# Kernel optimization log

Hardware: AMD Instinct MI355X
Metric: run time of the kernel (lower is better)

## Reference

```python
import jax, jax.numpy as jnp
import numpy as np

B, S, D = 2, 4096, 256
H, DH, DM = 8, 32, 1024
ROPE_BASE = 10000.0
LN_EPS = 1e-5


def _layer_norm(x, g, b):
    mu = jnp.mean(x, axis=-1, keepdims=True)
    var = jnp.mean(jnp.square(x - mu), axis=-1, keepdims=True)
    return (x - mu) * jax.lax.rsqrt(var + LN_EPS) * g + b


def _rope(x):
    # x: [b, s, h, d_head]; lucidrains interleaved-pair RoPE
    s, d = x.shape[1], x.shape[-1]
    inv_freq = 1.0 / (ROPE_BASE ** (jnp.arange(0, d, 2, dtype=jnp.float32) / d))  # [d/2]
    freqs = jnp.arange(s, dtype=jnp.float32)[:, None] * inv_freq[None, :]          # [s, d/2]
    freqs = jnp.repeat(freqs, 2, axis=-1)                                          # [s, d]
    cos = jnp.cos(freqs)[None, :, None, :]
    sin = jnp.sin(freqs)[None, :, None, :]
    x1, x2 = x[..., 0::2], x[..., 1::2]
    rot = jnp.stack((-x2, x1), axis=-1).reshape(x.shape)
    return x * cos + rot * sin


def setup_inputs() -> dict:
    key = jax.random.key(0)
    ks = jax.random.split(key, 8)
    sw = 1.0 / np.sqrt(D)
    return {
        "x": jax.random.normal(ks[0], (B, S, D), jnp.float32),
        "Wq": jax.random.normal(ks[1], (D, D), jnp.float32) * sw,
        "Wk": jax.random.normal(ks[2], (D, D), jnp.float32) * sw,
        "Wv": jax.random.normal(ks[3], (D, D), jnp.float32) * sw,
        "Wo": jax.random.normal(ks[4], (D, D), jnp.float32) * sw,
        "ln1_g": jnp.ones((D,), jnp.float32),
        "ln1_b": jnp.zeros((D,), jnp.float32),
        "ln2_g": jnp.ones((D,), jnp.float32),
        "ln2_b": jnp.zeros((D,), jnp.float32),
        "W2": jax.random.normal(ks[5], (DM, D), jnp.float32) * sw,
        "b2": jnp.zeros((DM,), jnp.float32),
        "W3": jax.random.normal(ks[6], (D, DM), jnp.float32) * (1.0 / np.sqrt(DM)),
        "b3": jnp.zeros((D,), jnp.float32),
    }


def reference(x, Wq, Wk, Wv, Wo, ln1_g, ln1_b, ln2_g, ln2_b, W2, b2, W3, b3):
    b, s, d = x.shape
    h, dh = H, DH
    xn = _layer_norm(x, ln1_g, ln1_b)
    q = (xn @ Wq.T).reshape(b, s, h, dh)
    k = (xn @ Wk.T).reshape(b, s, h, dh)
    v = (xn @ Wv.T).reshape(b, s, h, dh)
    q = _rope(q)
    k = _rope(k)
    # scores: [b, h, q, k] (full matrix, matching original implementation)
    scores = jnp.einsum('bqhd,bkhd->bhqk', q, k) / np.sqrt(dh)
    attn = jax.nn.softmax(scores, axis=-1)
    out = jnp.einsum('bhqk,bkhd->bqhd', attn, v).reshape(b, s, d)
    out = out @ Wo.T
    mlp_in = out + x
    y = _layer_norm(mlp_in, ln2_g, ln2_b)
    y = jax.nn.gelu(y @ W2.T + b2, approximate=False)
    y = y @ W3.T + b3
    return y + mlp_in
```

## Files before the change

kernel.cpp:

```cpp
#include <hip/hip_runtime.h>
#include <math.h>

#define D 256
#define S 4096
#define H 8
#define DH 32
#define DM 1024
#define NTOK 8192

typedef __attribute__((ext_vector_type(8))) short short8;
typedef __attribute__((ext_vector_type(4))) float f32x4;

#define QSCALE (0.17677669529663687f * 1.4426950408889634f)

__device__ inline unsigned short f2bf(float f) {
    union { float f; unsigned u; } v; v.f = f;
    unsigned r = v.u + 0x7fffu + ((v.u >> 16) & 1u);
    return (unsigned short)(r >> 16);
}
__device__ inline void gload16(const void* g, void* l) {
    __builtin_amdgcn_global_load_lds((const __attribute__((address_space(1))) void*)g,
                                     (__attribute__((address_space(3))) void*)l, 16, 0, 0);
}

__device__ inline short8 pack_p(f32x4 s0, f32x4 s1) {
    unsigned u0[4], u1[4];
    #pragma unroll
    for (int i = 0; i < 4; ++i) {
        union { float f; unsigned u; } c0, c1;
        c0.f = __builtin_amdgcn_exp2f(s0[i]);
        c1.f = __builtin_amdgcn_exp2f(s1[i]);
        u0[i] = c0.u;
        u1[i] = c1.u;
    }
    union { unsigned u[4]; short8 s; } pk;
    pk.u[0] = __builtin_amdgcn_perm(u0[1], u0[0], 0x07060302u);
    pk.u[1] = __builtin_amdgcn_perm(u0[3], u0[2], 0x07060302u);
    pk.u[2] = __builtin_amdgcn_perm(u1[1], u1[0], 0x07060302u);
    pk.u[3] = __builtin_amdgcn_perm(u1[3], u1[2], 0x07060302u);
    return pk.s;
}

__global__ void prep(const float* __restrict__ Wq, const float* __restrict__ Wk,
                     const float* __restrict__ Wv, const float* __restrict__ Wo,
                     const float* __restrict__ W2, const float* __restrict__ W3,
                     unsigned short* __restrict__ wqkv, unsigned short* __restrict__ wo_b,
                     unsigned short* __restrict__ w2_b, unsigned short* __restrict__ w3_b,
                     float* __restrict__ ct, float* __restrict__ st,
                     const float* __restrict__ x, const float* __restrict__ g,
                     const float* __restrict__ b, unsigned short* __restrict__ xn) {
    int blk = blockIdx.x;
    if (blk < 3328) {
        int i = blk * 256 + threadIdx.x;
        if (i < 196608) {
            const float* s = (i < 65536) ? Wq : ((i < 131072) ? Wk : Wv);
            wqkv[i] = f2bf(s[i & 65535]);
        } else if (i < 262144) {
            wo_b[i - 196608] = f2bf(Wo[i - 196608]);
        } else if (i < 524288) {
            w2_b[i - 262144] = f2bf(W2[i - 262144]);
        } else if (i < 786432) {
            w3_b[i - 524288] = f2bf(W3[i - 524288]);
        } else {
            int j = i - 786432;
            int spos = j >> 4, pi = j & 15;
            float inv_freq = powf(10000.0f, -(float)(2 * pi) / 32.0f);
            float fr = (float)spos * inv_freq;
            ct[j] = cosf(fr);
            st[j] = sinf(fr);
        }
        return;
    }
    int l = threadIdx.x & 63;
    int row = (blk - 3328) * 4 + (threadIdx.x >> 6);
    const float4 v = *(const float4*)(x + (size_t)row * D + l * 4);
    float s  = v.x + v.y + v.z + v.w;
    float s2 = v.x * v.x + v.y * v.y + v.z * v.z + v.w * v.w;
    #pragma unroll
    for (int off = 32; off > 0; off >>= 1) {
        s  += __shfl_xor(s, off, 64);
        s2 += __shfl_xor(s2, off, 64);
    }
    float mu  = s * (1.0f / D);
    float var = s2 * (1.0f / D) - mu * mu;
    float rs  = rsqrtf(var + 1e-5f);
    const float4 gg = *(const float4*)(g + l * 4);
    const float4 bb = *(const float4*)(b + l * 4);
    ushort4 o;
    o.x = f2bf((v.x - mu) * rs * gg.x + bb.x);
    o.y = f2bf((v.y - mu) * rs * gg.y + bb.y);
    o.z = f2bf((v.z - mu) * rs * gg.z + bb.z);
    o.w = f2bf((v.w - mu) * rs * gg.w + bb.w);
    *(ushort4*)(xn + (size_t)row * D + l * 4) = o;
}

__global__ void ln_kernel(const float* __restrict__ x, const float* __restrict__ g,
                          const float* __restrict__ b, unsigned short* __restrict__ out) {
    int l = threadIdx.x & 63;
    int row = blockIdx.x * 4 + (threadIdx.x >> 6);
    const float4 v = *(const float4*)(x + (size_t)row * D + l * 4);
    float s  = v.x + v.y + v.z + v.w;
    float s2 = v.x * v.x + v.y * v.y + v.z * v.z + v.w * v.w;
    #pragma unroll
    for (int off = 32; off > 0; off >>= 1) {
        s  += __shfl_xor(s, off, 64);
        s2 += __shfl_xor(s2, off, 64);
    }
    float mu  = s * (1.0f / D);
    float var = s2 * (1.0f / D) - mu * mu;
    float rs  = rsqrtf(var + 1e-5f);
    const float4 gg = *(const float4*)(g + l * 4);
    const float4 bb = *(const float4*)(b + l * 4);
    ushort4 o;
    o.x = f2bf((v.x - mu) * rs * gg.x + bb.x);
    o.y = f2bf((v.y - mu) * rs * gg.y + bb.y);
    o.z = f2bf((v.z - mu) * rs * gg.z + bb.z);
    o.w = f2bf((v.w - mu) * rs * gg.w + bb.w);
    *(ushort4*)(out + (size_t)row * D + l * 4) = o;
}

__global__ __launch_bounds__(256) void gemm64b(const unsigned short* __restrict__ A,
        const unsigned short* __restrict__ Bw, void* __restrict__ outp,
        unsigned short* __restrict__ vt,
        const float* __restrict__ bias,
        const float* __restrict__ ct, const float* __restrict__ st,
        int N, int K, int mode) {
    __shared__ unsigned short As[2][64 * 64];
    __shared__ unsigned short Bs[2][64 * 64];
    int tid = threadIdx.x;
    int w = tid >> 6, l = tid & 63;
    int lm = l & 15, lg = l >> 4;
    int wm = (w >> 1) * 32, wn = (w & 1) * 32;
    int bm = blockIdx.x * 64, bn = blockIdx.y * 64;
    int r1 = tid >> 3, pc = tid & 7;
    int pcx = (pc ^ (r1 & 7)) * 8;
    const unsigned short* Ag1 = A + (size_t)(bm + r1) * K + pcx;
    const unsigned short* Ag2 = A + (size_t)(bm + 32 + r1) * K + pcx;
    const unsigned short* Bg1 = Bw + (size_t)(bn + r1) * K + pcx;
    const unsigned short* Bg2 = Bw + (size_t)(bn + 32 + r1) * K + pcx;
    const int swz = lm & 7;
    f32x4 acc[2][2] = {};

    gload16(Ag1, &As[0][w * 512]);
    gload16(Ag2, &As[0][2048 + w * 512]);
    gload16(Bg1, &Bs[0][w * 512]);
    gload16(Bg2, &Bs[0][2048 + w * 512]);
    for (int k0 = 0; k0 < K; k0 += 64) {
        int cur = (k0 >> 6) & 1;
        __syncthreads();
        if (k0 + 64 < K) {
            gload16(Ag1 + k0 + 64, &As[1 - cur][w * 512]);
            gload16(Ag2 + k0 + 64, &As[1 - cur][2048 + w * 512]);
            gload16(Bg1 + k0 + 64, &Bs[1 - cur][w * 512]);
            gload16(Bg2 + k0 + 64, &Bs[1 - cur][2048 + w * 512]);
        }
        #pragma unroll
        for (int j = 0; j < 2; ++j) {
            int ch = ((j * 4 + lg) ^ swz) * 8;
            short8 af[2], bf[2];
            #pragma unroll
            for (int i = 0; i < 2; ++i) af[i] = *(const short8*)&As[cur][(wm + i * 16 + lm) * 64 + ch];
            #pragma unroll
            for (int i = 0; i < 2; ++i) bf[i] = *(const short8*)&Bs[cur][(wn + i * 16 + lm) * 64 + ch];
            #pragma unroll
            for (int mi = 0; mi < 2; ++mi)
                #pragma unroll
                for (int ni = 0; ni < 2; ++ni)
                    acc[mi][ni] = __builtin_amdgcn_mfma_f32_16x16x32_bf16(af[mi], bf[ni], acc[mi][ni], 0, 0, 0);
        }
    }

    if (mode == 0) {
        if (bn >= 512) {
            #pragma unroll
            for (int mi = 0; mi < 2; ++mi) {
                #pragma unroll
                for (int ni = 0; ni < 2; ++ni) {
                    int ng = bn + wn + ni * 16 + lm - 512;
                    int hh = ng >> 5, dh = ng & 31;
                    int mg0 = bm + wm + mi * 16 + lg * 4;
                    int bbx = mg0 >> 12, ss = mg0 & 4095;
                    ushort4 pv;
                    pv.x = f2bf(acc[mi][ni][0]); pv.y = f2bf(acc[mi][ni][1]);
                    pv.z = f2bf(acc[mi][ni][2]); pv.w = f2bf(acc[mi][ni][3]);
                    *(ushort4*)(vt + ((size_t)((bbx * 8 + hh) * 32 + dh)) * S + ss) = pv;
                }
            }
        } else {
            #pragma unroll
            for (int mi = 0; mi < 2; ++mi) {
                #pragma unroll
                for (int ni = 0; ni < 2; ++ni) {
                    int ng = bn + wn + ni * 16 + lm;
                    int pi = (ng & 31) >> 1;
                    float sgn = (ng & 1) ? 1.f : -1.f;
                    float qs  = (ng < 256) ? QSCALE : 1.f;
                    #pragma unroll
                    for (int r2 = 0; r2 < 4; ++r2) {
                        int mg = bm + wm + mi * 16 + lg * 4 + r2;
                        int spos = mg & (S - 1);
                        float vv = acc[mi][ni][r2];
                        float pv = __shfl_xor(vv, 1, 64);
                        float cs = ct[spos * 16 + pi];
                        float sn = st[spos * 16 + pi];
                        float ov = (vv * cs + sgn * pv * sn) * qs;
                        ((unsigned short*)outp)[(size_t)mg * N + ng] = f2bf(ov);
                    }
                }
            }
        }
        return;
    }
    #pragma unroll
    for (int mi = 0; mi < 2; ++mi) {
        #pragma unroll
        for (int ni = 0; ni < 2; ++ni) {
            int ng = bn + wn + ni * 16 + lm;
            #pragma unroll
            for (int r2 = 0; r2 < 4; ++r2) {
                int mg = bm + wm + mi * 16 + lg * 4 + r2;
                float t = acc[mi][ni][r2] + bias[ng];
                ((unsigned short*)outp)[(size_t)mg * N + ng] =
                    f2bf(0.5f * t * (1.0f + erff(t * 0.70710678118654752f)));
            }
        }
    }
}

__global__ __launch_bounds__(256) void gemm32(const unsigned short* __restrict__ A,
        const unsigned short* __restrict__ Bw, void* __restrict__ outp,
        const float* __restrict__ bias, const float* __restrict__ res,
        int N, int K, int mode) {
    __shared__ unsigned short As[2][64 * 128];
    __shared__ unsigned short Bs[2][64 * 128];
    int tid = threadIdx.x;
    int w = tid >> 6, l = tid & 63;
    int lm = l & 15, lg = l >> 4;
    int wm = (w >> 1) * 32, wn = (w & 1) * 32;
    int bm = blockIdx.x * 64, bn = blockIdx.y * 64;
    int r1 = tid >> 4, pc = tid & 15;
    int pcx = (pc ^ (r1 & 7)) * 8;
    const unsigned short* Ag1 = A + (size_t)(bm + r1) * K + pcx;
    const unsigned short* Ag2 = A + (size_t)(bm + 16 + r1) * K + pcx;
    const unsigned short* Ag3 = A + (size_t)(bm + 32 + r1) * K + pcx;
    const unsigned short* Ag4 = A + (size_t)(bm + 48 + r1) * K + pcx;
    const unsigned short* Bg1 = Bw + (size_t)(bn + r1) * K + pcx;
    const unsigned short* Bg2 = Bw + (size_t)(bn + 16 + r1) * K + pcx;
    const unsigned short* Bg3 = Bw + (size_t)(bn + 32 + r1) * K + pcx;
    const unsigned short* Bg4 = Bw + (size_t)(bn + 48 + r1) * K + pcx;
    const int swz = lm & 7;
    f32x4 acc[2][2] = {};

    gload16(Ag1, &As[0][w * 512]);
    gload16(Ag2, &As[0][2048 + w * 512]);
    gload16(Ag3, &As[0][4096 + w * 512]);
    gload16(Ag4, &As[0][6144 + w * 512]);
    gload16(Bg1, &Bs[0][w * 512]);
    gload16(Bg2, &Bs[0][2048 + w * 512]);
    gload16(Bg3, &Bs[0][4096 + w * 512]);
    gload16(Bg4, &Bs[0][6144 + w * 512]);
    for (int k0 = 0; k0 < K; k0 += 128) {
        int cur = (k0 >> 7) & 1;
        __syncthreads();
        if (k0 + 128 < K) {
            gload16(Ag1 + k0 + 128, &As[1 - cur][w * 512]);
            gload16(Ag2 + k0 + 128, &As[1 - cur][2048 + w * 512]);
            gload16(Ag3 + k0 + 128, &As[1 - cur][4096 + w * 512]);
            gload16(Ag4 + k0 + 128, &As[1 - cur][6144 + w * 512]);
            gload16(Bg1 + k0 + 128, &Bs[1 - cur][w * 512]);
            gload16(Bg2 + k0 + 128, &Bs[1 - cur][2048 + w * 512]);
            gload16(Bg3 + k0 + 128, &Bs[1 - cur][4096 + w * 512]);
            gload16(Bg4 + k0 + 128, &Bs[1 - cur][6144 + w * 512]);
        }
        #pragma unroll
        for (int j = 0; j < 4; ++j) {
            int ch = ((j * 4 + lg) ^ swz) * 8;
            short8 af[2], bf[2];
            #pragma unroll
            for (int i = 0; i < 2; ++i) af[i] = *(const short8*)&As[cur][(wm + i * 16 + lm) * 128 + ch];
            #pragma unroll
            for (int i = 0; i < 2; ++i) bf[i] = *(const short8*)&Bs[cur][(wn + i * 16 + lm) * 128 + ch];
            #pragma unroll
            for (int mi = 0; mi < 2; ++mi)
                #pragma unroll
                for (int ni = 0; ni < 2; ++ni)
                    acc[mi][ni] = __builtin_amdgcn_mfma_f32_16x16x32_bf16(af[mi], bf[ni], acc[mi][ni], 0, 0, 0);
        }
    }

    #pragma unroll
    for (int mi = 0; mi < 2; ++mi) {
        #pragma unroll
        for (int ni = 0; ni < 2; ++ni) {
            int ng = bn + wn + ni * 16 + lm;
            #pragma unroll
            for (int r2 = 0; r2 < 4; ++r2) {
                int mg = bm + wm + mi * 16 + lg * 4 + r2;
                float v = acc[mi][ni][r2];
                size_t idx = (size_t)mg * N + ng;
                if (mode == 1) {
                    ((float*)outp)[idx] = v + res[idx];
                } else {
                    ((float*)outp)[idx] = v + bias[ng] + res[idx];
                }
            }
        }
    }
}

__global__ __launch_bounds__(512, 4) void attn_kernel(const unsigned short* __restrict__ Cq,
        const unsigned short* __restrict__ vt, unsigned short* __restrict__ out) {
    __shared__ unsigned short Ks[2][3][64][32];
    __shared__ unsigned short Vs[2][3][32][64];
    int tid = threadIdx.x;
    int w = tid >> 6, l = tid & 63;
    int grp = w >> 2, ws = w & 3;
    int lm = l & 15, lg = l >> 4;
    int qt = blockIdx.x >> 4;
    int bh = blockIdx.x & 15;
    int bb = bh >> 3, h = bh & 7;
    int q0 = qt * 128 + ws * 32;

    const short8 qfa = *(const short8*)(Cq + ((size_t)(bb * S + q0 + lm)) * 768 + h * DH + lg * 8);
    const short8 qfb = *(const short8*)(Cq + ((size_t)(bb * S + q0 + 16 + lm)) * 768 + h * DH + lg * 8);

    union { unsigned short us[8]; short8 s; } onesu;
    {
        unsigned short ov = (lm == 0) ? (unsigned short)0x3F80 : (unsigned short)0;
        #pragma unroll
        for (int i = 0; i < 8; ++i) onesu.us[i] = ov;
    }
    const short8 onef = onesu.s;

    int p = ws * 16 + (l >> 2);
    int krow = ((p >> 5) << 5) + (((p >> 2) & 3) << 3) + (((p >> 4) & 1) << 2) + (p & 3);
    const unsigned short* kg = Cq + ((size_t)(bb * S)) * 768 + 256 + h * 32
                               + (size_t)krow * 768 + ((l & 3) ^ ((l >> 3) & 3)) * 8;
    const unsigned short* vg = vt + ((size_t)(bh * 32 + ws * 8 + (l >> 3))) * S + ((l & 7) ^ (l >> 3)) * 8;
    const int kswz = (lm >> 1) & 3;
    const int vswz = lm & 7;

    f32x4 o0a = {0.f, 0.f, 0.f, 0.f}, o1a = {0.f, 0.f, 0.f, 0.f}, o2a = {0.f, 0.f, 0.f, 0.f};
    f32x4 o0b = {0.f, 0.f, 0.f, 0.f}, o1b = {0.f, 0.f, 0.f, 0.f}, o2b = {0.f, 0.f, 0.f, 0.f};
    const f32x4 z = {0.f, 0.f, 0.f, 0.f};

    gload16(kg + (size_t)grp * 64 * 768,       &Ks[grp][0][ws * 16][0]);
    gload16(vg + (size_t)grp * 64,             &Vs[grp][0][ws * 8][0]);
    gload16(kg + (size_t)(2 + grp) * 64 * 768, &Ks[grp][1][ws * 16][0]);
    gload16(vg + (size_t)(2 + grp) * 64,       &Vs[grp][1][ws * 8][0]);
    asm volatile("s_waitcnt vmcnt(4)" ::: "memory");

#define ATTN_STEP(J, CUR, NXT) do {                                                          \
    asm volatile("s_waitcnt vmcnt(2) lgkmcnt(0)" ::: "memory");                              \
    __builtin_amdgcn_s_barrier();                                                            \
    __builtin_amdgcn_sched_barrier(0);                                                       \
    int tt_ = (J) + 2; if (tt_ > 31) tt_ = 31;                                               \
    size_t tg_ = (size_t)(2 * tt_ + grp);                                                    \
    gload16(kg + tg_ * 64 * 768, &Ks[grp][NXT][ws * 16][0]);                                 \
    gload16(vg + tg_ * 64,       &Vs[grp][NXT][ws * 8][0]);                                  \
    short8 kf0 = *(const short8*)&Ks[grp][CUR][lm][(lg ^ kswz) * 8];                         \
    short8 kf1 = *(const short8*)&Ks[grp][CUR][16 + lm][(lg ^ kswz) * 8];                    \
    short8 kf2 = *(const short8*)&Ks[grp][CUR][32 + lm][(lg ^ kswz) * 8];                    \
    short8 kf3 = *(const short8*)&Ks[grp][CUR][48 + lm][(lg ^ kswz) * 8];                    \
    __builtin_amdgcn_s_setprio(1);                                                           \
    f32x4 s0a = __builtin_amdgcn_mfma_f32_16x16x32_bf16(kf0, qfa, z, 0, 0, 0);               \
    f32x4 s1a = __builtin_amdgcn_mfma_f32_16x16x32_bf16(kf1, qfa, z, 0, 0, 0);               \
    f32x4 s0b = __builtin_amdgcn_mfma_f32_16x16x32_bf16(kf0, qfb, z, 0, 0, 0);               \
    f32x4 s1b = __builtin_amdgcn_mfma_f32_16x16x32_bf16(kf1, qfb, z, 0, 0, 0);               \
    f32x4 t0a = __builtin_amdgcn_mfma_f32_16x16x32_bf16(kf2, qfa, z, 0, 0, 0);               \
    f32x4 t1a = __builtin_amdgcn_mfma_f32_16x16x32_bf16(kf3, qfa, z, 0, 0, 0);               \
    f32x4 t0b = __builtin_amdgcn_mfma_f32_16x16x32_bf16(kf2, qfb, z, 0, 0, 0);               \
    f32x4 t1b = __builtin_amdgcn_mfma_f32_16x16x32_bf16(kf3, qfb, z, 0, 0, 0);               \
    __builtin_amdgcn_s_setprio(0);                                                           \
    short8 pfa = pack_p(s0a, s1a);                                                           \
    short8 pfb = pack_p(s0b, s1b);                                                           \
    int vc0 = (lg ^ vswz) * 8;                                                               \
    short8 va0 = *(const short8*)&Vs[grp][CUR][lm][vc0];                                     \
    short8 va1 = *(const short8*)&Vs[grp][CUR][16 + lm][vc0];                                \
    __builtin_amdgcn_s_setprio(1);                                                           \
    o0a = __builtin_amdgcn_mfma_f32_16x16x32_bf16(va0, pfa, o0a, 0, 0, 0);                   \
    o1a = __builtin_amdgcn_mfma_f32_16x16x32_bf16(va1, pfa, o1a, 0, 0, 0);                   \
    o2a = __builtin_amdgcn_mfma_f32_16x16x32_bf16(onef, pfa, o2a, 0, 0, 0);                  \
    o0b = __builtin_amdgcn_mfma_f32_16x16x32_bf16(va0, pfb, o0b, 0, 0, 0);                   \
    o1b = __builtin_amdgcn_mfma_f32_16x16x32_bf16(va1, pfb, o1b, 0, 0, 0);                   \
    o2b = __builtin_amdgcn_mfma_f32_16x16x32_bf16(onef, pfb, o2b, 0, 0, 0);                  \
    __builtin_amdgcn_s_setprio(0);                                                           \
    short8 pfa2 = pack_p(t0a, t1a);                                                          \
    short8 pfb2 = pack_p(t0b, t1b);                                                          \
    int vc1 = ((4 + lg) ^ vswz) * 8;                                                         \
    short8 vb0 = *(const short8*)&Vs[grp][CUR][lm][vc1];                                     \
    short8 vb1 = *(const short8*)&Vs[grp][CUR][16 + lm][vc1];                                \
    __builtin_amdgcn_s_setprio(1);                                                           \
    o0a = __builtin_amdgcn_mfma_f32_16x16x32_bf16(vb0, pfa2, o0a, 0, 0, 0);                  \
    o1a = __builtin_amdgcn_mfma_f32_16x16x32_bf16(vb1, pfa2, o1a, 0, 0, 0);                  \
    o2a = __builtin_amdgcn_mfma_f32_16x16x32_bf16(onef, pfa2, o2a, 0, 0, 0);                 \
    o0b = __builtin_amdgcn_mfma_f32_16x16x32_bf16(vb0, pfb2, o0b, 0, 0, 0);                  \
    o1b = __builtin_amdgcn_mfma_f32_16x16x32_bf16(vb1, pfb2, o1b, 0, 0, 0);                  \
    o2b = __builtin_amdgcn_mfma_f32_16x16x32_bf16(onef, pfb2, o2b, 0, 0, 0);                 \
    __builtin_amdgcn_s_setprio(0);                                                           \
} while (0)

    for (int j3 = 0; j3 < 30; j3 += 3) {
        ATTN_STEP(j3,     0, 2);
        ATTN_STEP(j3 + 1, 1, 0);
        ATTN_STEP(j3 + 2, 2, 1);
    }
    ATTN_STEP(30, 0, 2);
    ATTN_STEP(31, 1, 0);
#undef ATTN_STEP

    f32x4* Red = (f32x4*)&Ks[0][0][0][0];
    float* Den = (float*)&Vs[0][0][0][0];
    __syncthreads();
    if (grp) {
        Red[(0 * 4 + ws) * 64 + l] = o0a;
        Red[(1 * 4 + ws) * 64 + l] = o1a;
        Red[(2 * 4 + ws) * 64 + l] = o0b;
        Red[(3 * 4 + ws) * 64 + l] = o1b;
        Den[(ws * 2 + 0) * 64 + l] = o2a[0];
        Den[(ws * 2 + 1) * 64 + l] = o2b[0];
    }
    __syncthreads();
    if (!grp) {
        f32x4 a0 = Red[(0 * 4 + ws) * 64 + l];
        f32x4 a1 = Red[(1 * 4 + ws) * 64 + l];
        f32x4 a2 = Red[(2 * 4 + ws) * 64 + l];
        f32x4 a3 = Red[(3 * 4 + ws) * 64 + l];
        float dda = o2a[0] + Den[(ws * 2 + 0) * 64 + l];
        float ddb = o2b[0] + Den[(ws * 2 + 1) * 64 + l];
        #pragma unroll
        for (int i = 0; i < 4; ++i) {
            o0a[i] += a0[i]; o1a[i] += a1[i];
            o0b[i] += a2[i]; o1b[i] += a3[i];
        }
        float inva = 1.0f / __shfl(dda, lm, 64);
        float invb = 1.0f / __shfl(ddb, lm, 64);
        ushort4 r0, r1;
        r0.x = f2bf(o0a[0] * inva); r0.y = f2bf(o0a[1] * inva);
        r0.z = f2bf(o0a[2] * inva); r0.w = f2bf(o0a[3] * inva);
        r1.x = f2bf(o1a[0] * inva); r1.y = f2bf(o1a[1] * inva);
        r1.z = f2bf(o1a[2] * inva); r1.w = f2bf(o1a[3] * inva);
        unsigned short* ob = out + ((size_t)(bb * S + q0 + lm)) * D + h * DH;
        *(ushort4*)(ob + lg * 4)      = r0;
        *(ushort4*)(ob + 16 + lg * 4) = r1;
        r0.x = f2bf(o0b[0] * invb); r0.y = f2bf(o0b[1] * invb);
        r0.z = f2bf(o0b[2] * invb); r0.w = f2bf(o0b[3] * invb);
        r1.x = f2bf(o1b[0] * invb); r1.y = f2bf(o1b[1] * invb);
        r1.z = f2bf(o1b[2] * invb); r1.w = f2bf(o1b[3] * invb);
        unsigned short* ob2 = out + ((size_t)(bb * S + q0 + 16 + lm)) * D + h * DH;
        *(ushort4*)(ob2 + lg * 4)      = r0;
        *(ushort4*)(ob2 + 16 + lg * 4) = r1;
    }
}

extern "C" void kernel_launch(void* const* d_in, const int* in_sizes, int n_in,
                              void* d_out, int out_size, void* d_ws, size_t ws_size,
                              hipStream_t stream) {
    const float* x     = (const float*)d_in[0];
    const float* Wq    = (const float*)d_in[1];
    const float* Wk    = (const float*)d_in[2];
    const float* Wv    = (const float*)d_in[3];
    const float* Wo    = (const float*)d_in[4];
    const float* ln1_g = (const float*)d_in[5];
    const float* ln1_b = (const float*)d_in[6];
    const float* ln2_g = (const float*)d_in[7];
    const float* ln2_b = (const float*)d_in[8];
    const float* W2    = (const float*)d_in[9];
    const float* b2    = (const float*)d_in[10];
    const float* W3    = (const float*)d_in[11];
    const float* b3    = (const float*)d_in[12];

    char* w8 = (char*)d_ws;
    unsigned short* wqkv = (unsigned short*)(w8);
    unsigned short* wo_b = (unsigned short*)(w8 + 393216);
    unsigned short* w2_b = (unsigned short*)(w8 + 524288);
    unsigned short* w3_b = (unsigned short*)(w8 + 1048576);
    float*          ct   = (float*)(w8 + 1572864);
    float*          st   = (float*)(w8 + 1835008);
    unsigned short* xn   = (unsigned short*)(w8 + 2097152);
    unsigned short* Cq   = (unsigned short*)(w8 + 6291456);
    unsigned short* hb   = Cq;
    unsigned short* vtb  = (unsigned short*)(w8 + 23068672);
    unsigned short* ab   = (unsigned short*)(w8 + 27262976);
    float*          mlpin= (float*)(w8 + 31457280);
    unsigned short* yn   = xn;

    prep<<<5376, 256, 0, stream>>>(Wq, Wk, Wv, Wo, W2, W3, wqkv, wo_b, w2_b, w3_b,
                                   ct, st, x, ln1_g, ln1_b, xn);
    gemm64b<<<dim3(128, 12), 256, 0, stream>>>(xn, wqkv, Cq, vtb, nullptr, ct, st, 768, 256, 0);
    attn_kernel<<<512, 512, 0, stream>>>(Cq, vtb, ab);
    gemm32<<<dim3(128, 4), 256, 0, stream>>>(ab, wo_b, mlpin, nullptr, x, 256, 256, 1);
    ln_kernel<<<NTOK / 4, 256, 0, stream>>>(mlpin, ln2_g, ln2_b, yn);
    gemm64b<<<dim3(128, 16), 256, 0, stream>>>(yn, w2_b, hb, nullptr, b2, nullptr, nullptr, 1024, 256, 2);
    gemm32<<<dim3(128, 4), 256, 0, stream>>>(hb, w3_b, (float*)d_out, b3, mlpin, 256, 1024, 3);
}
```

Baseline: 180.3 us.

## Triple-buffer gemm32 with 64-wide K tiles and explicit vmcnt waits

The 64x64 output GEMM now uses K tiles of 64 instead of 128 and a three-stage LDS ring buffer, prefetching two tiles ahead. A partial s_waitcnt vmcnt(4) plus a raw s_barrier replaces the full __syncthreads, so loads for later stages stay in flight while the current tile is consumed. This cuts LDS per block (3x8KB per matrix instead of 2x16KB), which may raise occupancy. In exchange the loop runs twice as many iterations with more barriers, and the final iterations issue redundant clamped loads.

```diff
diff --git a/kernel.cpp b/kernel.cpp
--- a/kernel.cpp
+++ b/kernel.cpp
@@ -231,55 +231,52 @@
         const unsigned short* __restrict__ Bw, void* __restrict__ outp,
         const float* __restrict__ bias, const float* __restrict__ res,
         int N, int K, int mode) {
-    __shared__ unsigned short As[2][64 * 128];
-    __shared__ unsigned short Bs[2][64 * 128];
+    __shared__ unsigned short As[3][64 * 64];
+    __shared__ unsigned short Bs[3][64 * 64];
     int tid = threadIdx.x;
     int w = tid >> 6, l = tid & 63;
     int lm = l & 15, lg = l >> 4;
     int wm = (w >> 1) * 32, wn = (w & 1) * 32;
     int bm = blockIdx.x * 64, bn = blockIdx.y * 64;
-    int r1 = tid >> 4, pc = tid & 15;
+    int r1 = tid >> 3, pc = tid & 7;
     int pcx = (pc ^ (r1 & 7)) * 8;
     const unsigned short* Ag1 = A + (size_t)(bm + r1) * K + pcx;
-    const unsigned short* Ag2 = A + (size_t)(bm + 16 + r1) * K + pcx;
-    const unsigned short* Ag3 = A + (size_t)(bm + 32 + r1) * K + pcx;
-    const unsigned short* Ag4 = A + (size_t)(bm + 48 + r1) * K + pcx;
+    const unsigned short* Ag2 = A + (size_t)(bm + 32 + r1) * K + pcx;
     const unsigned short* Bg1 = Bw + (size_t)(bn + r1) * K + pcx;
-    const unsigned short* Bg2 = Bw + (size_t)(bn + 16 + r1) * K + pcx;
-    const unsigned short* Bg3 = Bw + (size_t)(bn + 32 + r1) * K + pcx;
-    const unsigned short* Bg4 = Bw + (size_t)(bn + 48 + r1) * K + pcx;
+    const unsigned short* Bg2 = Bw + (size_t)(bn + 32 + r1) * K + pcx;
     const int swz = lm & 7;
     f32x4 acc[2][2] = {};
-
-    gload16(Ag1, &As[0][w * 512]);
-    gload16(Ag2, &As[0][2048 + w * 512]);
-    gload16(Ag3, &As[0][4096 + w * 512]);
-    gload16(Ag4, &As[0][6144 + w * 512]);
-    gload16(Bg1, &Bs[0][w * 512]);
-    gload16(Bg2, &Bs[0][2048 + w * 512]);
-    gload16(Bg3, &Bs[0][4096 + w * 512]);
-    gload16(Bg4, &Bs[0][6144 + w * 512]);
-    for (int k0 = 0; k0 < K; k0 += 128) {
-        int cur = (k0 >> 7) & 1;
-        __syncthreads();
-        if (k0 + 128 < K) {
-            gload16(Ag1 + k0 + 128, &As[1 - cur][w * 512]);
-            gload16(Ag2 + k0 + 128, &As[1 - cur][2048 + w * 512]);
-            gload16(Ag3 + k0 + 128, &As[1 - cur][4096 + w * 512]);
-            gload16(Ag4 + k0 + 128, &As[1 - cur][6144 + w * 512]);
-            gload16(Bg1 + k0 + 128, &Bs[1 - cur][w * 512]);
-            gload16(Bg2 + k0 + 128, &Bs[1 - cur][2048 + w * 512]);
-            gload16(Bg3 + k0 + 128, &Bs[1 - cur][4096 + w * 512]);
-            gload16(Bg4 + k0 + 128, &Bs[1 - cur][6144 + w * 512]);
-        }
-        #pragma unroll
-        for (int j = 0; j < 4; ++j) {
+    const int nk = K >> 6;
+
+    gload16(Ag1,      &As[0][w * 512]);
+    gload16(Ag2,      &As[0][2048 + w * 512]);
+    gload16(Bg1,      &Bs[0][w * 512]);
+    gload16(Bg2,      &Bs[0][2048 + w * 512]);
+    gload16(Ag1 + 64, &As[1][w * 512]);
+    gload16(Ag2 + 64, &As[1][2048 + w * 512]);
+    gload16(Bg1 + 64, &Bs[1][w * 512]);
+    gload16(Bg2 + 64, &Bs[1][2048 + w * 512]);
+
+    for (int it = 0; it < nk; ++it) {
+        int cur = it % 3;
+        int nxt = (it + 2) % 3;
+        asm volatile("s_waitcnt vmcnt(4) lgkmcnt(0)" ::: "memory");
+        __builtin_amdgcn_s_barrier();
+        __builtin_amdgcn_sched_barrier(0);
+        int tn = it + 2; if (tn > nk - 1) tn = nk - 1;
+        int ko = tn << 6;
+        gload16(Ag1 + ko, &As[nxt][w * 512]);
+        gload16(Ag2 + ko, &As[nxt][2048 + w * 512]);
+        gload16(Bg1 + ko, &Bs[nxt][w * 512]);
+        gload16(Bg2 + ko, &Bs[nxt][2048 + w * 512]);
+        #pragma unroll
+        for (int j = 0; j < 2; ++j) {
             int ch = ((j * 4 + lg) ^ swz) * 8;
             short8 af[2], bf[2];
             #pragma unroll
-            for (int i = 0; i < 2; ++i) af[i] = *(const short8*)&As[cur][(wm + i * 16 + lm) * 128 + ch];
-            #pragma unroll
-            for (int i = 0; i < 2; ++i) bf[i] = *(const short8*)&Bs[cur][(wn + i * 16 + lm) * 128 + ch];
+            for (int i = 0; i < 2; ++i) af[i] = *(const short8*)&As[cur][(wm + i * 16 + lm) * 64 + ch];
+            #pragma unroll
+            for (int i = 0; i < 2; ++i) bf[i] = *(const short8*)&Bs[cur][(wn + i * 16 + lm) * 64 + ch];
             #pragma unroll
             for (int mi = 0; mi < 2; ++mi)
                 #pragma unroll
@@ -287,6 +284,7 @@
                     acc[mi][ni] = __builtin_amdgcn_mfma_f32_16x16x32_bf16(af[mi], bf[ni], acc[mi][ni], 0, 0, 0);
         }
     }
+    asm volatile("s_waitcnt vmcnt(0)" ::: "memory");
 
     #pragma unroll
     for (int mi = 0; mi < 2; ++mi) {
```

After: 185.4 us. 1.03x slower.
